# Optimization experiments

Measured on AMD Instinct MI355X. Metric: run time of the kernel, lower is better.

## Reference

```python
import jax, jax.numpy as jnp
import numpy as np
from jax import lax

V_JOINTS = 25
N_SCALES = 13
C1 = 96
N_SEG = 50
EPS = 1e-5

# NTU RGB+D 25-joint skeleton edges (0-indexed)
_EDGES = [(0,1),(1,20),(2,20),(3,2),(4,20),(5,4),(6,5),(7,6),(8,20),(9,8),
          (10,9),(11,10),(12,0),(13,12),(14,13),(15,14),(16,0),(17,16),
          (18,17),(19,18),(21,22),(22,7),(23,24),(24,11)]


def _build_A_powers():
    # MS-G3D disentangled multi-scale adjacency: k-hop shells, D^-1/2 A D^-1/2 normalized
    A = np.zeros((V_JOINTS, V_JOINTS), dtype=np.float64)
    for i, j in _EDGES:
        A[i, j] = 1.0
        A[j, i] = 1.0
    I = np.eye(V_JOINTS)
    mats = []
    for k in range(N_SCALES):
        if k == 0:
            Ak = I.copy()
        else:
            Ak = (np.minimum(np.linalg.matrix_power(A + I, k), 1)
                  - np.minimum(np.linalg.matrix_power(A + I, k - 1), 1))
            Ak = Ak + I  # with_self=True
        d = Ak.sum(-1)
        Dinv = np.diag(d ** -0.5)
        mats.append(Dinv @ Ak @ Dinv)
    return np.concatenate(mats, axis=0).astype(np.float32)  # (13*25, 25)


def _segments(T, n_seg):
    # Segment boundaries exactly as the torch code: int(round(linspace(1, T, n_seg+1)))
    t_vec = [int(round(v)) for v in np.linspace(1, T, n_seg + 1)]
    lens = [t_vec[i + 1] - t_vec[i] for i in range(n_seg)]
    L = max(lens)
    idx = np.zeros((n_seg, L), dtype=np.int32)
    mask = np.zeros((n_seg, L), dtype=np.float32)
    for s in range(n_seg):
        start = t_vec[s] - 1
        for l in range(L):
            idx[s, l] = min(start + l, T - 2)
            mask[s, l] = 1.0 if l < lens[s] else 0.0
    sp_idx = np.array([t - 1 for t in t_vec[:-1]], dtype=np.int32)
    return idx, mask, sp_idx


def setup_inputs() -> dict:
    key = jax.random.key(0)
    ks = jax.random.split(key, 18)
    N, M, C, T, V = 4, 2, 3, 300, V_JOINTS
    num_classes = 60
    Cbn = M * C * V                       # 150
    Dlog = C1 + C1 * (C1 - 1) // 2        # 4656 (depth-2 logsig dims)
    Din = C1 + Dlog                       # 4752 (start pos + logsig)
    f = lambda k, s: jax.random.normal(k, s, dtype=jnp.float32)
    return {
        'x': f(ks[0], (N, M, C, T, V)),
        'bn_g': 1.0 + 0.1 * f(ks[1], (Cbn,)),
        'bn_b': 0.1 * f(ks[2], (Cbn,)),
        'bn_m': 0.1 * f(ks[3], (Cbn,)),
        'bn_v': jax.random.uniform(ks[4], (Cbn,), minval=0.5, maxval=1.5),
        'A_powers': jnp.asarray(_build_A_powers()),
        'A_res': jax.random.uniform(ks[5], (N_SCALES * V, V), minval=-1e-6, maxval=1e-6),
        'W_gcn': f(ks[6], (C1, N_SCALES * C)) / np.sqrt(N_SCALES * C),
        'b_gcn': 0.1 * f(ks[7], (C1,)),
        'bn2_g': 1.0 + 0.1 * f(ks[8], (C1,)),
        'bn2_b': 0.1 * f(ks[9], (C1,)),
        'bn2_m': 0.1 * f(ks[10], (C1,)),
        'bn2_v': jax.random.uniform(ks[11], (C1,), minval=0.5, maxval=1.5),
        'W_ih': f(ks[12], (4 * C1, Din)) / np.sqrt(Din),
        'W_hh': f(ks[13], (4 * C1, C1)) / np.sqrt(C1),
        'b_ih': 0.1 * f(ks[14], (4 * C1,)),
        'b_hh': 0.1 * f(ks[15], (4 * C1,)),
        'W_fc': f(ks[16], (num_classes, C1)) / np.sqrt(C1),
        'b_fc': 0.1 * f(ks[17], (num_classes,)),
    }


def reference(x, bn_g, bn_b, bn_m, bn_v, A_powers, A_res, W_gcn, b_gcn,
              bn2_g, bn2_b, bn2_m, bn2_v, W_ih, W_hh, b_ih, b_hh, W_fc, b_fc):
    N, M, C, T, V = x.shape
    NM = N * M
    # --- data_bn (inference BatchNorm1d over M*V*C channels) ---
    xb = x.transpose(0, 1, 4, 2, 3).reshape(N, M * V * C, T)
    xb = (xb - bn_m[:, None]) * (bn_g / jnp.sqrt(bn_v + EPS))[:, None] + bn_b[:, None]
    xg = xb.reshape(NM, V, C, T).transpose(0, 2, 3, 1)          # (NM, C, T, V)
    # --- MS_GCN: multi-scale disentangled graph conv ---
    A = A_powers + A_res                                        # (S*V, V)
    sup = jnp.einsum('vu,nctu->nctv', A, xg)                    # (NM, C, T, S*V)
    sup = sup.reshape(NM, C, T, N_SCALES, V).transpose(0, 3, 1, 2, 4)
    sup = sup.reshape(NM, N_SCALES * C, T, V)
    y = jnp.einsum('oc,nctv->notv', W_gcn, sup) + b_gcn[None, :, None, None]
    y = (y - bn2_m[None, :, None, None]) * (bn2_g / jnp.sqrt(bn2_v + EPS))[None, :, None, None] \
        + bn2_b[None, :, None, None]
    y = jax.nn.relu(y)                                          # (NM, C1, T, V)
    # --- LogSigRNN: per-joint temporal path, depth-2 log-signature per segment ---
    p = y.transpose(0, 3, 2, 1).reshape(NM * V, T, C1)          # (B, T, C1)
    idx, mask, sp_idx = _segments(T, N_SEG)
    dx = jnp.diff(p, axis=1)                                    # (B, T-1, C1)
    dseg = dx[:, idx] * mask[None, :, :, None]                  # (B, nseg, L, C1)
    pseg = jnp.cumsum(dseg, axis=2) - dseg                      # exclusive prefix within segment
    s1 = dseg.sum(axis=2)                                       # level-1: total increment
    Q = jnp.einsum('bslc,bsld->bscd', pseg, dseg)               # (B, nseg, C1, C1)
    levy = 0.5 * (Q - jnp.swapaxes(Q, -1, -2))                  # level-2 (Levy area)
    iu, ju = np.triu_indices(C1, 1)
    ls2 = levy[:, :, iu, ju]                                    # (B, nseg, 4560)
    start_pos = p[:, sp_idx, :]                                 # (B, nseg, C1)
    feat = jnp.concatenate([start_pos, s1, ls2], axis=-1)       # (B, nseg, 4752)
    # --- LSTM (torch gate order i,f,g,o) ---
    B = feat.shape[0]
    xw = jnp.einsum('btd,gd->btg', feat, W_ih) + (b_ih + b_hh)
    def step(carry, xt):
        h, c = carry
        g = xt + h @ W_hh.T
        i, fg, gg, o = jnp.split(g, 4, axis=-1)
        c = jax.nn.sigmoid(fg) * c + jax.nn.sigmoid(i) * jnp.tanh(gg)
        h = jax.nn.sigmoid(o) * jnp.tanh(c)
        return (h, c), h
    h0 = jnp.zeros((B, C1), feat.dtype)
    _, hs = lax.scan(step, (h0, h0), jnp.swapaxes(xw, 0, 1))
    hs = jnp.swapaxes(hs, 0, 1)                                 # (B, nseg, C1)
    out = hs.reshape(NM, V, N_SEG, C1).transpose(0, 3, 2, 1)    # (NM, C1, nseg, V)
    out = out.reshape(N, M, C1, -1).mean(axis=3).mean(axis=1)   # (N, C1)
    return out @ W_fc.T + b_fc
```

## Files before the change

kernel.cpp:

```cpp
#include <hip/hip_runtime.h>
#include <math.h>

#define KF 4752
#define KP 4768
#define KSTEPS 149
#define G4 384
#define NPAIR 4560
#define EPSBN 1e-5f
#define XWHALF 3840000

typedef float f32x4 __attribute__((ext_vector_type(4)));
typedef short s16x8 __attribute__((ext_vector_type(8)));

__device__ __forceinline__ unsigned short f2bf(float x){
  unsigned u = __float_as_uint(x);
  return (unsigned short)((u + 0x7fffu + ((u>>16)&1u)) >> 16);
}
__device__ __forceinline__ float bf2f(unsigned short h){
  return __uint_as_float(((unsigned)h)<<16);
}

__device__ __forceinline__ int seg_start(int s){ return (s<=24)? 6*s : 149 + 6*(s-25); }
__device__ __forceinline__ int seg_len(int s){ return (s==24)?5:6; }

__global__ void kGeff(const float* bn_g, const float* bn_v,
                      const float* Ap, const float* Ar, const float* Wg,
                      const float* bn2_g, const float* bn2_v, float* geffT){
  int idx = blockIdx.x*256 + threadIdx.x;
  if (idx >= 2*96*25*75) return;
  int cu = idx % 75; int rest = idx/75;
  int v = rest % 25; rest /= 25;
  int o = rest % 96; int m = rest / 96;
  int c = cu/25, u = cu%25;
  int ch = (m*25+u)*3 + c;
  float s1 = bn_g[ch] / sqrtf(bn_v[ch] + EPSBN);
  float s2 = bn2_g[o] / sqrtf(bn2_v[o] + EPSBN);
  float acc = 0.f;
  for (int k=0;k<13;k++){
    float a = Ap[(k*25+v)*25+u] + Ar[(k*25+v)*25+u];
    acc += Wg[o*39 + k*3 + c] * a;
  }
  geffT[((size_t)(m*75+cu))*2400 + v*96 + o] = acc * s1 * s2;
}

__global__ __launch_bounds__(256) void kBeff(const float* bn_g,const float* bn_b,const float* bn_m,const float* bn_v,
                      const float* Ap,const float* Ar,const float* Wg,const float* bg,
                      const float* bn2_g,const float* bn2_b,const float* bn2_m,const float* bn2_v,
                      float* beffT){
  int wid  = (blockIdx.x*256 + threadIdx.x) >> 6;
  int lane = threadIdx.x & 63;
  if (wid >= 2*96*25) return;
  int v = wid % 25; int rest = wid/25; int o = rest % 96; int m = rest/96;
  float acc = 0.f;
  #pragma unroll
  for (int it=0; it<16; ++it){
    int item = it*64 + lane;
    if (item < 975){
      int k = item / 75; int cu = item % 75; int c = cu/25, u = cu%25;
      int ch = (m*25+u)*3 + c;
      float s1 = bn_g[ch] / sqrtf(bn_v[ch] + EPSBN);
      float t1 = bn_b[ch] - bn_m[ch]*s1;
      float a  = Ap[(k*25+v)*25+u] + Ar[(k*25+v)*25+u];
      acc += Wg[o*39 + k*3 + c] * a * t1;
    }
  }
  #pragma unroll
  for (int off=32; off; off>>=1) acc += __shfl_down(acc, off);
  if (lane == 0){
    acc += bg[o];
    float s2 = bn2_g[o]/sqrtf(bn2_v[o]+EPSBN);
    beffT[m*2400 + v*96 + o] = s2*(acc - bn2_m[o]) + bn2_b[o];
  }
}

__global__ void kPairs(int* pairs){
  int k = blockIdx.x*256+threadIdx.x;
  if (k >= NPAIR) return;
  int i=0, rem=k;
  while (rem >= 95 - i){ rem -= (95 - i); i++; }
  int j = i + 1 + rem;
  pairs[k] = (i<<7) | j;
}

__global__ void kWsplit(const float* w, unsigned short* whi, unsigned short* wlo){
  int idx = blockIdx.x*256 + threadIdx.x;
  if (idx >= G4*KP) return;
  int g = idx / KP, k = idx % KP;
  float v = (k < KF) ? w[(size_t)g*KF + k] : 0.f;
  unsigned short h = f2bf(v);
  whi[idx] = h;
  wlo[idx] = f2bf(v - bf2f(h));
}

#define TTILE 10
__global__ __launch_bounds__(256) void kP(const float* x, const float* geffT, const float* beffT, float* p){
  int nm = blockIdx.y;
  int t0 = blockIdx.x * TTILE;
  int m  = nm % 2;
  __shared__ float xs[75*TTILE];
  int tid = threadIdx.x;
  for (int li = tid; li < 75*TTILE; li += 256){
    int u = li % 25; int rest = li/25; int tt = rest % TTILE; int c = rest / TTILE;
    xs[(c*25+u)*TTILE + tt] = x[(((size_t)nm*3 + c)*300 + (t0+tt))*25 + u];
  }
  __syncthreads();
  const float* gT = geffT + (size_t)m*75*2400;
  for (int ow = tid; ow < 2400; ow += 256){
    int o = ow % 96, v = ow / 96;
    float b = beffT[m*2400 + ow];
    float acc[TTILE];
    #pragma unroll
    for (int t=0;t<TTILE;t++) acc[t] = b;
    for (int cu=0; cu<75; cu++){
      float gv = gT[(size_t)cu*2400 + ow];
      #pragma unroll
      for (int t=0;t<TTILE;t++) acc[t] += gv * xs[cu*TTILE+t];
    }
    #pragma unroll
    for (int t=0;t<TTILE;t++)
      p[((size_t)(nm*25+v)*300 + t0+t)*96 + o] = fmaxf(acc[t], 0.f);
  }
}

__global__ __launch_bounds__(256) void kFeat(const float* p, const int* pairs,
                                             unsigned short* fhi, unsigned short* flo, int row0){
  int row = row0 + blockIdx.x;
  int b = row / 50, s = row % 50;
  int S = seg_start(s), len = seg_len(s);
  __shared__ float ps[6][96];
  __shared__ float ds[6][96];
  int tid = threadIdx.x;
  size_t base = (size_t)blockIdx.x * KP;
  if (tid < 96){
    int c = tid;
    float pv[7];
    #pragma unroll
    for (int l=0;l<7;l++) pv[l] = p[((size_t)b*300 + S + l)*96 + c];
    float run = 0.f;
    #pragma unroll
    for (int l=0;l<6;l++){
      float d = (l < len) ? (pv[l+1]-pv[l]) : 0.f;
      ps[l][c] = run; ds[l][c] = d; run += d;
    }
    unsigned short h0 = f2bf(pv[0]);
    fhi[base + c] = h0; flo[base + c] = f2bf(pv[0] - bf2f(h0));
    unsigned short h1 = f2bf(run);
    fhi[base + 96 + c] = h1; flo[base + 96 + c] = f2bf(run - bf2f(h1));
  } else if (tid < 112){
    int c = KF + (tid - 96);
    fhi[base + c] = 0; flo[base + c] = 0;
  }
  __syncthreads();
  for (int k = tid; k < NPAIR; k += 256){
    int pr = pairs[k];
    int i = pr >> 7, j = pr & 127;
    float q = 0.f;
    #pragma unroll
    for (int l=0;l<6;l++) q += ps[l][i]*ds[l][j] - ps[l][j]*ds[l][i];
    q *= 0.5f;
    unsigned short h = f2bf(q);
    fhi[base + 192 + k] = h; flo[base + 192 + k] = f2bf(q - bf2f(h));
  }
}

__device__ __forceinline__ void gload16(const void* g, void* l){
  __builtin_amdgcn_global_load_lds(
      (const __attribute__((address_space(1))) void*)g,
      (__attribute__((address_space(3))) void*)l, 16, 0, 0);
}

__global__ __launch_bounds__(256) void kGemm(
    const unsigned short* __restrict__ fhi, const unsigned short* __restrict__ flo,
    const unsigned short* __restrict__ whi, const unsigned short* __restrict__ wlo,
    float* __restrict__ xw, int chunkRow0, int nrows)
{
  __shared__ unsigned short lds[2][20480];
  int tid  = threadIdx.x;
  int lane = tid & 63, w = tid >> 6;
  int colBase = blockIdx.x * 192;
  int zz      = blockIdx.y;
  int mblk    = blockIdx.z;
  int zbase   = zz * 75;
  int zSteps  = zz ? (KSTEPS - 75) : 75;

  const unsigned short* gptr[10];
  int ldsOff[10];
  #pragma unroll
  for (int q=0;q<10;q++){
    int c = (w*10 + q)*64 + lane;
    const unsigned short* bp; int rr;
    if (c < 512)        { rr = c;        bp = fhi + (size_t)(mblk*128 + (rr>>2))*KP; }
    else if (c < 1024)  { rr = c-512;    bp = flo + (size_t)(mblk*128 + (rr>>2))*KP; }
    else if (c < 1792)  { rr = c-1024;   bp = whi + (size_t)(colBase  + (rr>>2))*KP; }
    else                { rr = c-1792;   bp = wlo + (size_t)(colBase  + (rr>>2))*KP; }
    int row = rr>>2, gl = rr&3;
    int gs = gl ^ ((row>>1)&3);
    gptr[q]  = bp + gs*8;
    ldsOff[q] = (w*10 + q)*512;
  }

  int wm = w & 1, wn = w >> 1;
  int gsel = lane >> 4;
  int aoff[4], boff[6];
  #pragma unroll
  for (int fm=0; fm<4; fm++){
    int r = wm*64 + fm*16 + (lane&15);
    aoff[fm] = r*32 + ((gsel ^ ((r>>1)&3))*8);
  }
  #pragma unroll
  for (int fn=0; fn<6; fn++){
    int r = wn*96 + fn*16 + (lane&15);
    boff[fn] = 8192 + r*32 + ((gsel ^ ((r>>1)&3))*8);
  }

  f32x4 acc[4][6];
  #pragma unroll
  for (int fm=0;fm<4;fm++)
    #pragma unroll
    for (int fn=0;fn<6;fn++) acc[fm][fn] = (f32x4){0.f,0.f,0.f,0.f};

  #pragma unroll
  for (int q=0;q<10;q++) gload16(gptr[q] + (size_t)zbase*32, &lds[0][ldsOff[q]]);

  int cur = 0;
  for (int t=0; t<zSteps; ++t){
    __syncthreads();
    if (t+1 < zSteps){
      size_t ko = (size_t)(zbase + t + 1)*32;
      #pragma unroll
      for (int q=0;q<10;q++) gload16(gptr[q] + ko, &lds[cur^1][ldsOff[q]]);
    }
    const unsigned short* L = lds[cur];
    s16x8 ah[4], al[4], bh[6], bl[6];
    #pragma unroll
    for (int fm=0;fm<4;fm++){
      ah[fm] = *(const s16x8*)(L + aoff[fm]);
      al[fm] = *(const s16x8*)(L + aoff[fm] + 4096);
    }
    #pragma unroll
    for (int fn=0;fn<6;fn++){
      bh[fn] = *(const s16x8*)(L + boff[fn]);
      bl[fn] = *(const s16x8*)(L + boff[fn] + 6144);
    }
    #pragma unroll
    for (int fm=0;fm<4;fm++)
      #pragma unroll
      for (int fn=0;fn<6;fn++){
        acc[fm][fn] = __builtin_amdgcn_mfma_f32_16x16x32_bf16(ah[fm], bh[fn], acc[fm][fn], 0,0,0);
        acc[fm][fn] = __builtin_amdgcn_mfma_f32_16x16x32_bf16(ah[fm], bl[fn], acc[fm][fn], 0,0,0);
        acc[fm][fn] = __builtin_amdgcn_mfma_f32_16x16x32_bf16(al[fm], bh[fn], acc[fm][fn], 0,0,0);
      }
    cur ^= 1;
  }

  int rl = (lane>>4)*4, cl = lane&15;
  float* outp = xw + (size_t)zz*XWHALF;
  #pragma unroll
  for (int fm=0;fm<4;fm++){
    #pragma unroll
    for (int fn=0;fn<6;fn++){
      int gr0 = mblk*128 + wm*64 + fm*16 + rl;
      int gc  = colBase + wn*96 + fn*16 + cl;
      f32x4 v = acc[fm][fn];
      #pragma unroll
      for (int r=0;r<4;r++){
        int gr = gr0 + r;
        if (gr < nrows)
          outp[(size_t)(chunkRow0 + gr)*G4 + gc] = v[r];
      }
    }
  }
}

__global__ __launch_bounds__(384) void kLstm(const float* xw, const float* whh,
                                             const float* bih, const float* bhh, float* hsum){
  int b = blockIdx.x;
  int g = threadIdx.x;
  __shared__ __align__(16) float h_s[96];
  __shared__ float gbuf[384];
  float wreg[96];
  #pragma unroll
  for (int k=0;k<96;k++) wreg[k] = whh[(size_t)g*96 + k];
  float breg = bih[g] + bhh[g];
  float cval = 0.f, hacc = 0.f;
  if (g < 96) h_s[g] = 0.f;
  __syncthreads();
  const float* xrow  = xw + (size_t)b*50*G4;
  const float* xrow2 = xrow + XWHALF;
  for (int t=0;t<50;t++){
    float acc = xrow[t*G4 + g] + xrow2[t*G4 + g] + breg;
    #pragma unroll
    for (int k=0;k<96;k+=4){
      float4 h4 = *(const float4*)&h_s[k];
      acc += wreg[k]*h4.x + wreg[k+1]*h4.y + wreg[k+2]*h4.z + wreg[k+3]*h4.w;
    }
    gbuf[g] = acc;
    __syncthreads();
    if (g < 96){
      float ig = gbuf[g], fg = gbuf[96+g], gg = gbuf[192+g], og = gbuf[288+g];
      float si = 1.f/(1.f+expf(-ig));
      float sf = 1.f/(1.f+expf(-fg));
      float so = 1.f/(1.f+expf(-og));
      cval = sf*cval + si*tanhf(gg);
      float h = so * tanhf(cval);
      h_s[g] = h;
      hacc += h;
    }
    __syncthreads();
  }
  if (g < 96) hsum[(size_t)b*96 + g] = hacc;
}

__global__ void kOut(const float* hsum, const float* wfc, const float* bfc, float* out){
  int n = blockIdx.x;
  __shared__ float pool[96];
  int tid = threadIdx.x;
  if (tid < 96){
    float a = 0.f;
    for (int mv=0; mv<50; mv++) a += hsum[((size_t)(n*50 + mv))*96 + tid];
    pool[tid] = a / 2500.f;
  }
  __syncthreads();
  if (tid < 60){
    float a = bfc[tid];
    for (int o=0;o<96;o++) a += pool[o]*wfc[tid*96+o];
    out[n*60+tid] = a;
  }
}

extern "C" void kernel_launch(void* const* d_in, const int* in_sizes, int n_in,
                              void* d_out, int out_size, void* d_ws, size_t ws_size,
                              hipStream_t stream){
  const float* x     = (const float*)d_in[0];
  const float* bn_g  = (const float*)d_in[1];
  const float* bn_b  = (const float*)d_in[2];
  const float* bn_m  = (const float*)d_in[3];
  const float* bn_v  = (const float*)d_in[4];
  const float* Ap    = (const float*)d_in[5];
  const float* Ar    = (const float*)d_in[6];
  const float* Wg    = (const float*)d_in[7];
  const float* bg    = (const float*)d_in[8];
  const float* bn2_g = (const float*)d_in[9];
  const float* bn2_b = (const float*)d_in[10];
  const float* bn2_m = (const float*)d_in[11];
  const float* bn2_v = (const float*)d_in[12];
  const float* wih   = (const float*)d_in[13];
  const float* whh   = (const float*)d_in[14];
  const float* bih   = (const float*)d_in[15];
  const float* bhh   = (const float*)d_in[16];
  const float* wfc   = (const float*)d_in[17];
  const float* bfc   = (const float*)d_in[18];
  float* out = (float*)d_out;

  float* ws    = (float*)d_ws;
  float* geffT = ws;
  float* beffT = geffT + 360000;
  int*   pairs = (int*)(beffT + 4800);
  float* pbuf  = beffT + 4800 + 4560;
  float* xw    = pbuf + 5760000;
  float* hsum  = xw + 2*XWHALF;
  unsigned short* whiP = (unsigned short*)(hsum + 19200);
  unsigned short* wloP = whiP + (size_t)G4*KP;
  unsigned short* fhi  = wloP + (size_t)G4*KP;
  size_t fixedFloats = 360000u + 4800u + 4560u + 5760000u + 2u*XWHALF + 19200u
                     + (size_t)G4*KP;
  long long availB = (long long)ws_size - (long long)(fixedFloats*4);
  long long perBlk128 = 128LL*KP*2*2;
  int blocks128 = (availB > 0) ? (int)(availB / perBlk128) : 1;
  if (blocks128 < 1)  blocks128 = 1;
  if (blocks128 > 79) blocks128 = 79;
  int chunkRows = blocks128 * 128;
  unsigned short* flo = fhi + (size_t)chunkRows*KP;

  kGeff<<<(2*96*25*75 + 255)/256, 256, 0, stream>>>(bn_g, bn_v, Ap, Ar, Wg, bn2_g, bn2_v, geffT);
  kBeff<<<1200, 256, 0, stream>>>(bn_g, bn_b, bn_m, bn_v, Ap, Ar, Wg, bg,
                                  bn2_g, bn2_b, bn2_m, bn2_v, beffT);
  kPairs<<<(NPAIR + 255)/256, 256, 0, stream>>>(pairs);
  kWsplit<<<((G4*KP) + 255)/256, 256, 0, stream>>>(wih, whiP, wloP);
  kP<<<dim3(30, 8), 256, 0, stream>>>(x, geffT, beffT, pbuf);

  for (int r0 = 0; r0 < 10000; r0 += chunkRows){
    int nr = 10000 - r0; if (nr > chunkRows) nr = chunkRows;
    kFeat<<<nr, 256, 0, stream>>>(pbuf, pairs, fhi, flo, r0);
    kGemm<<<dim3(2, 2, (nr + 127)/128), 256, 0, stream>>>(fhi, flo, whiP, wloP, xw, r0, nr);
  }

  kLstm<<<200, 384, 0, stream>>>(xw, whh, bih, bhh, hsum);
  kOut<<<4, 128, 0, stream>>>(hsum, wfc, bfc, out);
}
```

Measured before the change: 397.7 us.

## Enlarge GEMM M-tile, remap blocks to XCDs, fuse prep kernels, vectorize feature writes

```diff
diff --git a/kernel.cpp b/kernel.cpp
--- a/kernel.cpp
+++ b/kernel.cpp
@@ -23,73 +23,76 @@
 __device__ __forceinline__ int seg_start(int s){ return (s<=24)? 6*s : 149 + 6*(s-25); }
 __device__ __forceinline__ int seg_len(int s){ return (s==24)?5:6; }
 
-__global__ void kGeff(const float* bn_g, const float* bn_v,
-                      const float* Ap, const float* Ar, const float* Wg,
-                      const float* bn2_g, const float* bn2_v, float* geffT){
-  int idx = blockIdx.x*256 + threadIdx.x;
-  if (idx >= 2*96*25*75) return;
-  int cu = idx % 75; int rest = idx/75;
-  int v = rest % 25; rest /= 25;
-  int o = rest % 96; int m = rest / 96;
-  int c = cu/25, u = cu%25;
-  int ch = (m*25+u)*3 + c;
-  float s1 = bn_g[ch] / sqrtf(bn_v[ch] + EPSBN);
-  float s2 = bn2_g[o] / sqrtf(bn2_v[o] + EPSBN);
-  float acc = 0.f;
-  for (int k=0;k<13;k++){
-    float a = Ap[(k*25+v)*25+u] + Ar[(k*25+v)*25+u];
-    acc += Wg[o*39 + k*3 + c] * a;
-  }
-  geffT[((size_t)(m*75+cu))*2400 + v*96 + o] = acc * s1 * s2;
-}
-
-__global__ __launch_bounds__(256) void kBeff(const float* bn_g,const float* bn_b,const float* bn_m,const float* bn_v,
-                      const float* Ap,const float* Ar,const float* Wg,const float* bg,
-                      const float* bn2_g,const float* bn2_b,const float* bn2_m,const float* bn2_v,
-                      float* beffT){
-  int wid  = (blockIdx.x*256 + threadIdx.x) >> 6;
-  int lane = threadIdx.x & 63;
-  if (wid >= 2*96*25) return;
-  int v = wid % 25; int rest = wid/25; int o = rest % 96; int m = rest/96;
-  float acc = 0.f;
-  #pragma unroll
-  for (int it=0; it<16; ++it){
-    int item = it*64 + lane;
-    if (item < 975){
-      int k = item / 75; int cu = item % 75; int c = cu/25, u = cu%25;
-      int ch = (m*25+u)*3 + c;
-      float s1 = bn_g[ch] / sqrtf(bn_v[ch] + EPSBN);
-      float t1 = bn_b[ch] - bn_m[ch]*s1;
-      float a  = Ap[(k*25+v)*25+u] + Ar[(k*25+v)*25+u];
-      acc += Wg[o*39 + k*3 + c] * a * t1;
-    }
-  }
-  #pragma unroll
-  for (int off=32; off; off>>=1) acc += __shfl_down(acc, off);
-  if (lane == 0){
-    acc += bg[o];
-    float s2 = bn2_g[o]/sqrtf(bn2_v[o]+EPSBN);
-    beffT[m*2400 + v*96 + o] = s2*(acc - bn2_m[o]) + bn2_b[o];
-  }
-}
-
-__global__ void kPairs(int* pairs){
-  int k = blockIdx.x*256+threadIdx.x;
-  if (k >= NPAIR) return;
-  int i=0, rem=k;
-  while (rem >= 95 - i){ rem -= (95 - i); i++; }
-  int j = i + 1 + rem;
-  pairs[k] = (i<<7) | j;
-}
-
-__global__ void kWsplit(const float* w, unsigned short* whi, unsigned short* wlo){
-  int idx = blockIdx.x*256 + threadIdx.x;
-  if (idx >= G4*KP) return;
-  int g = idx / KP, k = idx % KP;
-  float v = (k < KF) ? w[(size_t)g*KF + k] : 0.f;
-  unsigned short h = f2bf(v);
-  whi[idx] = h;
-  wlo[idx] = f2bf(v - bf2f(h));
+#define NB_GEFF 1407
+#define NB_BEFF 1200
+#define NB_PAIR 18
+#define NB_WSPL 7152
+
+__global__ __launch_bounds__(256) void kPre(
+    const float* bn_g,const float* bn_b,const float* bn_m,const float* bn_v,
+    const float* Ap,const float* Ar,const float* Wg,const float* bg,
+    const float* bn2_g,const float* bn2_b,const float* bn2_m,const float* bn2_v,
+    const float* wih,
+    float* geffT, float* beffT, int* pairs, unsigned short* whi, unsigned short* wlo)
+{
+  int bid = blockIdx.x, tid = threadIdx.x;
+  if (bid < NB_GEFF){
+    int idx = bid*256 + tid;
+    if (idx >= 2*96*25*75) return;
+    int cu = idx % 75; int rest = idx/75;
+    int v = rest % 25; rest /= 25;
+    int o = rest % 96; int m = rest / 96;
+    int c = cu/25, u = cu%25;
+    int ch = (m*25+u)*3 + c;
+    float s1 = bn_g[ch] / sqrtf(bn_v[ch] + EPSBN);
+    float s2 = bn2_g[o] / sqrtf(bn2_v[o] + EPSBN);
+    float acc = 0.f;
+    for (int k=0;k<13;k++){
+      float a = Ap[(k*25+v)*25+u] + Ar[(k*25+v)*25+u];
+      acc += Wg[o*39 + k*3 + c] * a;
+    }
+    geffT[((size_t)(m*75+cu))*2400 + v*96 + o] = acc * s1 * s2;
+  } else if (bid < NB_GEFF + NB_BEFF){
+    int wid  = ((bid-NB_GEFF)*256 + tid) >> 6;
+    int lane = tid & 63;
+    if (wid >= 2*96*25) return;
+    int v = wid % 25; int rest = wid/25; int o = rest % 96; int m = rest/96;
+    float acc = 0.f;
+    #pragma unroll
+    for (int it=0; it<16; ++it){
+      int item = it*64 + lane;
+      if (item < 975){
+        int k = item / 75; int cu = item % 75; int c = cu/25, u = cu%25;
+        int ch = (m*25+u)*3 + c;
+        float s1 = bn_g[ch] / sqrtf(bn_v[ch] + EPSBN);
+        float t1 = bn_b[ch] - bn_m[ch]*s1;
+        float a  = Ap[(k*25+v)*25+u] + Ar[(k*25+v)*25+u];
+        acc += Wg[o*39 + k*3 + c] * a * t1;
+      }
+    }
+    #pragma unroll
+    for (int off=32; off; off>>=1) acc += __shfl_down(acc, off);
+    if (lane == 0){
+      acc += bg[o];
+      float s2 = bn2_g[o]/sqrtf(bn2_v[o]+EPSBN);
+      beffT[m*2400 + v*96 + o] = s2*(acc - bn2_m[o]) + bn2_b[o];
+    }
+  } else if (bid < NB_GEFF + NB_BEFF + NB_PAIR){
+    int k = (bid - NB_GEFF - NB_BEFF)*256 + tid;
+    if (k >= NPAIR) return;
+    int i=0, rem=k;
+    while (rem >= 95 - i){ rem -= (95 - i); i++; }
+    int j = i + 1 + rem;
+    pairs[k] = (i<<7) | j;
+  } else {
+    int idx = (bid - NB_GEFF - NB_BEFF - NB_PAIR)*256 + tid;
+    if (idx >= G4*KP) return;
+    int g = idx / KP, k = idx % KP;
+    float v = (k < KF) ? wih[(size_t)g*KF + k] : 0.f;
+    unsigned short h = f2bf(v);
+    whi[idx] = h;
+    wlo[idx] = f2bf(v - bf2f(h));
+  }
 }
 
 #define TTILE 10
@@ -127,8 +130,8 @@
   int row = row0 + blockIdx.x;
   int b = row / 50, s = row % 50;
   int S = seg_start(s), len = seg_len(s);
-  __shared__ float ps[6][96];
-  __shared__ float ds[6][96];
+  __shared__ float ps8[96][12];
+  __shared__ float ds8[96][12];
   int tid = threadIdx.x;
   size_t base = (size_t)blockIdx.x * KP;
   if (tid < 96){
@@ -140,8 +143,9 @@
     #pragma unroll
     for (int l=0;l<6;l++){
       float d = (l < len) ? (pv[l+1]-pv[l]) : 0.f;
-      ps[l][c] = run; ds[l][c] = d; run += d;
-    }
+      ps8[c][l] = run; ds8[c][l] = d; run += d;
+    }
+    ps8[c][6] = 0.f; ps8[c][7] = 0.f; ds8[c][6] = 0.f; ds8[c][7] = 0.f;
     unsigned short h0 = f2bf(pv[0]);
     fhi[base + c] = h0; flo[base + c] = f2bf(pv[0] - bf2f(h0));
     unsigned short h1 = f2bf(run);
@@ -151,15 +155,32 @@
     fhi[base + c] = 0; flo[base + c] = 0;
   }
   __syncthreads();
-  for (int k = tid; k < NPAIR; k += 256){
-    int pr = pairs[k];
-    int i = pr >> 7, j = pr & 127;
-    float q = 0.f;
-    #pragma unroll
-    for (int l=0;l<6;l++) q += ps[l][i]*ds[l][j] - ps[l][j]*ds[l][i];
-    q *= 0.5f;
-    unsigned short h = f2bf(q);
-    fhi[base + 192 + k] = h; flo[base + 192 + k] = f2bf(q - bf2f(h));
+  for (int g8 = tid; g8 < NPAIR/8; g8 += 256){
+    int k0 = g8*8;
+    s16x8 vh, vl;
+    int icur = -1;
+    f32x4 pi0={0,0,0,0}, pi1={0,0,0,0}, di0={0,0,0,0}, di1={0,0,0,0};
+    #pragma unroll
+    for (int e=0;e<8;e++){
+      int pr = pairs[k0+e]; int i = pr>>7, j = pr&127;
+      if (i != icur){
+        icur = i;
+        pi0 = *(const f32x4*)&ps8[i][0]; pi1 = *(const f32x4*)&ps8[i][4];
+        di0 = *(const f32x4*)&ds8[i][0]; di1 = *(const f32x4*)&ds8[i][4];
+      }
+      f32x4 pj0 = *(const f32x4*)&ps8[j][0], pj1 = *(const f32x4*)&ps8[j][4];
+      f32x4 dj0 = *(const f32x4*)&ds8[j][0], dj1 = *(const f32x4*)&ds8[j][4];
+      float q = pi0.x*dj0.x + pi0.y*dj0.y + pi0.z*dj0.z + pi0.w*dj0.w
+              + pi1.x*dj1.x + pi1.y*dj1.y
+              - pj0.x*di0.x - pj0.y*di0.y - pj0.z*di0.z - pj0.w*di0.w
+              - pj1.x*di1.x - pj1.y*di1.y;
+      q *= 0.5f;
+      unsigned short h = f2bf(q);
+      vh[e] = (short)h;
+      vl[e] = (short)f2bf(q - bf2f(h));
+    }
+    *(s16x8*)(fhi + base + 192 + k0) = vh;
+    *(s16x8*)(flo + base + 192 + k0) = vl;
   }
 }
 
@@ -172,94 +193,99 @@
 __global__ __launch_bounds__(256) void kGemm(
     const unsigned short* __restrict__ fhi, const unsigned short* __restrict__ flo,
     const unsigned short* __restrict__ whi, const unsigned short* __restrict__ wlo,
-    float* __restrict__ xw, int chunkRow0, int nrows)
+    float* __restrict__ xw, int chunkRow0, int nrows, int nmblk)
 {
-  __shared__ unsigned short lds[2][20480];
+  __shared__ unsigned short lds[2][28672];
   int tid  = threadIdx.x;
   int lane = tid & 63, w = tid >> 6;
-  int colBase = blockIdx.x * 192;
-  int zz      = blockIdx.y;
-  int mblk    = blockIdx.z;
-  int zbase   = zz * 75;
-  int zSteps  = zz ? (KSTEPS - 75) : 75;
-
-  const unsigned short* gptr[10];
-  int ldsOff[10];
-  #pragma unroll
-  for (int q=0;q<10;q++){
-    int c = (w*10 + q)*64 + lane;
-    const unsigned short* bp; int rr;
-    if (c < 512)        { rr = c;        bp = fhi + (size_t)(mblk*128 + (rr>>2))*KP; }
-    else if (c < 1024)  { rr = c-512;    bp = flo + (size_t)(mblk*128 + (rr>>2))*KP; }
-    else if (c < 1792)  { rr = c-1024;   bp = whi + (size_t)(colBase  + (rr>>2))*KP; }
-    else                { rr = c-1792;   bp = wlo + (size_t)(colBase  + (rr>>2))*KP; }
-    int row = rr>>2, gl = rr&3;
-    int gs = gl ^ ((row>>1)&3);
-    gptr[q]  = bp + gs*8;
-    ldsOff[q] = (w*10 + q)*512;
+  int id = blockIdx.x;
+  int col, zz, mblk;
+  if (nmblk == 40){
+    int xcd = id & 7, rank = id >> 3, s2 = rank >> 1;
+    col = rank & 1;
+    int pp = s2*8 + xcd;
+    mblk = pp >> 1; zz = pp & 1;
+  } else { col = id & 1; zz = (id >> 1) & 1; mblk = id >> 2; }
+  int rowBase = mblk*256, colBase = col*192;
+  int zbase = zz*75, zSteps = zz ? 74 : 75;
+
+  int off[14];
+  #pragma unroll
+  for (int q=0;q<14;q++){
+    int c = q*256 + tid;
+    int rr = (q<4) ? c : (q<8) ? c-1024 : (q<11) ? c-2048 : c-2816;
+    int rw = rr>>2, gl = rr&3;
+    int gs = gl ^ ((rw>>1)&3);
+    int grow = (q<8) ? (rowBase + rw) : (colBase + rw);
+    off[q] = grow*KP + gs*8;
   }
 
   int wm = w & 1, wn = w >> 1;
-  int gsel = lane >> 4;
-  int aoff[4], boff[6];
-  #pragma unroll
-  for (int fm=0; fm<4; fm++){
-    int r = wm*64 + fm*16 + (lane&15);
+  int gsel = lane >> 4, li = lane & 15;
+  int aoff[8], boff[6];
+  #pragma unroll
+  for (int fm=0; fm<8; fm++){
+    int r = wm*128 + fm*16 + li;
     aoff[fm] = r*32 + ((gsel ^ ((r>>1)&3))*8);
   }
   #pragma unroll
   for (int fn=0; fn<6; fn++){
-    int r = wn*96 + fn*16 + (lane&15);
-    boff[fn] = 8192 + r*32 + ((gsel ^ ((r>>1)&3))*8);
-  }
-
-  f32x4 acc[4][6];
-  #pragma unroll
-  for (int fm=0;fm<4;fm++)
+    int r = wn*96 + fn*16 + li;
+    boff[fn] = 16384 + r*32 + ((gsel ^ ((r>>1)&3))*8);
+  }
+
+  f32x4 acc[8][6];
+  #pragma unroll
+  for (int fm=0;fm<8;fm++)
     #pragma unroll
     for (int fn=0;fn<6;fn++) acc[fm][fn] = (f32x4){0.f,0.f,0.f,0.f};
 
-  #pragma unroll
-  for (int q=0;q<10;q++) gload16(gptr[q] + (size_t)zbase*32, &lds[0][ldsOff[q]]);
-
-  int cur = 0;
-  for (int t=0; t<zSteps; ++t){
-    __syncthreads();
-    if (t+1 < zSteps){
-      size_t ko = (size_t)(zbase + t + 1)*32;
-      #pragma unroll
-      for (int q=0;q<10;q++) gload16(gptr[q] + ko, &lds[cur^1][ldsOff[q]]);
-    }
-    const unsigned short* L = lds[cur];
-    s16x8 ah[4], al[4], bh[6], bl[6];
-    #pragma unroll
-    for (int fm=0;fm<4;fm++){
-      ah[fm] = *(const s16x8*)(L + aoff[fm]);
-      al[fm] = *(const s16x8*)(L + aoff[fm] + 4096);
-    }
-    #pragma unroll
-    for (int fn=0;fn<6;fn++){
-      bh[fn] = *(const s16x8*)(L + boff[fn]);
-      bl[fn] = *(const s16x8*)(L + boff[fn] + 6144);
-    }
-    #pragma unroll
-    for (int fm=0;fm<4;fm++)
-      #pragma unroll
-      for (int fn=0;fn<6;fn++){
-        acc[fm][fn] = __builtin_amdgcn_mfma_f32_16x16x32_bf16(ah[fm], bh[fn], acc[fm][fn], 0,0,0);
-        acc[fm][fn] = __builtin_amdgcn_mfma_f32_16x16x32_bf16(ah[fm], bl[fn], acc[fm][fn], 0,0,0);
-        acc[fm][fn] = __builtin_amdgcn_mfma_f32_16x16x32_bf16(al[fm], bh[fn], acc[fm][fn], 0,0,0);
-      }
-    cur ^= 1;
-  }
+#define STAGE(BUF, T) { \
+    int ko = (zbase + (T))*32; \
+    _Pragma("unroll") \
+    for (int q=0;q<14;q++){ \
+      const unsigned short* bp = (q<4)?fhi:(q<8)?flo:(q<11)?whi:wlo; \
+      gload16(bp + (size_t)(off[q] + ko), &lds[BUF][q*2048 + w*512]); \
+    } }
+
+#define COMPUTE(BI) { \
+    const unsigned short* L = lds[BI]; \
+    s16x8 bh[6], bl[6]; \
+    _Pragma("unroll") \
+    for (int fn=0;fn<6;fn++){ \
+      bh[fn] = *(const s16x8*)(L + boff[fn]); \
+      bl[fn] = *(const s16x8*)(L + boff[fn] + 6144); \
+    } \
+    _Pragma("unroll") \
+    for (int fm=0;fm<8;fm++){ \
+      s16x8 ah = *(const s16x8*)(L + aoff[fm]); \
+      s16x8 al = *(const s16x8*)(L + aoff[fm] + 8192); \
+      _Pragma("unroll") \
+      for (int fn=0;fn<6;fn++){ \
+        acc[fm][fn] = __builtin_amdgcn_mfma_f32_16x16x32_bf16(ah, bh[fn], acc[fm][fn], 0,0,0); \
+        acc[fm][fn] = __builtin_amdgcn_mfma_f32_16x16x32_bf16(ah, bl[fn], acc[fm][fn], 0,0,0); \
+        acc[fm][fn] = __builtin_amdgcn_mfma_f32_16x16x32_bf16(al, bh[fn], acc[fm][fn], 0,0,0); \
+      } \
+    } }
+
+  STAGE(0, 0);
+  for (int t=0; t<zSteps-1; ++t){
+    __builtin_amdgcn_s_barrier();
+    STAGE((t+1)&1, t+1);
+    asm volatile("s_waitcnt vmcnt(14)" ::: "memory");
+    COMPUTE(t&1);
+  }
+  __builtin_amdgcn_s_barrier();
+  asm volatile("s_waitcnt vmcnt(0)" ::: "memory");
+  COMPUTE((zSteps-1)&1);
 
   int rl = (lane>>4)*4, cl = lane&15;
   float* outp = xw + (size_t)zz*XWHALF;
   #pragma unroll
-  for (int fm=0;fm<4;fm++){
+  for (int fm=0;fm<8;fm++){
     #pragma unroll
     for (int fn=0;fn<6;fn++){
-      int gr0 = mblk*128 + wm*64 + fm*16 + rl;
+      int gr0 = rowBase + wm*128 + fm*16 + rl;
       int gc  = colBase + wn*96 + fn*16 + cl;
       f32x4 v = acc[fm][fn];
       #pragma unroll
@@ -270,45 +296,52 @@
       }
     }
   }
-}
-
-__global__ __launch_bounds__(384) void kLstm(const float* xw, const float* whh,
+#undef STAGE
+#undef COMPUTE
+}
+
+__global__ __launch_bounds__(192) void kLstm(const float* xw, const float* whh,
                                              const float* bih, const float* bhh, float* hsum){
   int b = blockIdx.x;
-  int g = threadIdx.x;
+  int t = threadIdx.x;
+  int gA = t;
+  int gB = t + 192;
   __shared__ __align__(16) float h_s[96];
   __shared__ float gbuf[384];
-  float wreg[96];
-  #pragma unroll
-  for (int k=0;k<96;k++) wreg[k] = whh[(size_t)g*96 + k];
-  float breg = bih[g] + bhh[g];
+  float wA[96], wB[96];
+  #pragma unroll
+  for (int k=0;k<96;k++){ wA[k] = whh[(size_t)gA*96 + k]; wB[k] = whh[(size_t)gB*96 + k]; }
+  float bA = bih[gA] + bhh[gA];
+  float bB = bih[gB] + bhh[gB];
   float cval = 0.f, hacc = 0.f;
-  if (g < 96) h_s[g] = 0.f;
+  if (t < 96) h_s[t] = 0.f;
   __syncthreads();
-  const float* xrow  = xw + (size_t)b*50*G4;
-  const float* xrow2 = xrow + XWHALF;
-  for (int t=0;t<50;t++){
-    float acc = xrow[t*G4 + g] + xrow2[t*G4 + g] + breg;
+  const float* xr = xw + (size_t)b*50*G4;
+  for (int st=0; st<50; st++){
+    int o = st*G4;
+    float aA = xr[o+gA] + xr[XWHALF+o+gA] + bA;
+    float aB = xr[o+gB] + xr[XWHALF+o+gB] + bB;
     #pragma unroll
     for (int k=0;k<96;k+=4){
       float4 h4 = *(const float4*)&h_s[k];
-      acc += wreg[k]*h4.x + wreg[k+1]*h4.y + wreg[k+2]*h4.z + wreg[k+3]*h4.w;
-    }
-    gbuf[g] = acc;
+      aA += wA[k]*h4.x + wA[k+1]*h4.y + wA[k+2]*h4.z + wA[k+3]*h4.w;
+      aB += wB[k]*h4.x + wB[k+1]*h4.y + wB[k+2]*h4.z + wB[k+3]*h4.w;
+    }
+    gbuf[gA] = aA; gbuf[gB] = aB;
     __syncthreads();
-    if (g < 96){
-      float ig = gbuf[g], fg = gbuf[96+g], gg = gbuf[192+g], og = gbuf[288+g];
+    if (t < 96){
+      float ig = gbuf[t], fg = gbuf[96+t], gg = gbuf[192+t], og = gbuf[288+t];
       float si = 1.f/(1.f+expf(-ig));
       float sf = 1.f/(1.f+expf(-fg));
       float so = 1.f/(1.f+expf(-og));
       cval = sf*cval + si*tanhf(gg);
       float h = so * tanhf(cval);
-      h_s[g] = h;
+      h_s[t] = h;
       hacc += h;
     }
     __syncthreads();
   }
-  if (g < 96) hsum[(size_t)b*96 + g] = hacc;
+  if (t < 96) hsum[(size_t)b*96 + t] = hacc;
 }
 
 __global__ void kOut(const float* hsum, const float* wfc, const float* bfc, float* out){
@@ -358,33 +391,32 @@
   int*   pairs = (int*)(beffT + 4800);
   float* pbuf  = beffT + 4800 + 4560;
   float* xw    = pbuf + 5760000;
-  float* hsum  = xw + 2*XWHALF;
+  float* hsum  = xw + 2*(size_t)XWHALF;
   unsigned short* whiP = (unsigned short*)(hsum + 19200);
   unsigned short* wloP = whiP + (size_t)G4*KP;
   unsigned short* fhi  = wloP + (size_t)G4*KP;
-  size_t fixedFloats = 360000u + 4800u + 4560u + 5760000u + 2u*XWHALF + 19200u
+  size_t fixedFloats = 360000u + 4800u + 4560u + 5760000u + 2u*(size_t)XWHALF + 19200u
                      + (size_t)G4*KP;
   long long availB = (long long)ws_size - (long long)(fixedFloats*4);
-  long long perBlk128 = 128LL*KP*2*2;
-  int blocks128 = (availB > 0) ? (int)(availB / perBlk128) : 1;
-  if (blocks128 < 1)  blocks128 = 1;
-  if (blocks128 > 79) blocks128 = 79;
-  int chunkRows = blocks128 * 128;
-  unsigned short* flo = fhi + (size_t)chunkRows*KP;
-
-  kGeff<<<(2*96*25*75 + 255)/256, 256, 0, stream>>>(bn_g, bn_v, Ap, Ar, Wg, bn2_g, bn2_v, geffT);
-  kBeff<<<1200, 256, 0, stream>>>(bn_g, bn_b, bn_m, bn_v, Ap, Ar, Wg, bg,
-                                  bn2_g, bn2_b, bn2_m, bn2_v, beffT);
-  kPairs<<<(NPAIR + 255)/256, 256, 0, stream>>>(pairs);
-  kWsplit<<<((G4*KP) + 255)/256, 256, 0, stream>>>(wih, whiP, wloP);
+  long long perUnit = 256LL*KP*4;
+  long long units = (availB > 0) ? availB/perUnit : 1;
+  if (units < 1)  units = 1;
+  if (units > 40) units = 40;
+  int chunk = (int)units * 256;
+  unsigned short* flo = fhi + (size_t)chunk*KP;
+
+  kPre<<<NB_GEFF+NB_BEFF+NB_PAIR+NB_WSPL, 256, 0, stream>>>(
+      bn_g, bn_b, bn_m, bn_v, Ap, Ar, Wg, bg, bn2_g, bn2_b, bn2_m, bn2_v,
+      wih, geffT, beffT, pairs, whiP, wloP);
   kP<<<dim3(30, 8), 256, 0, stream>>>(x, geffT, beffT, pbuf);
 
-  for (int r0 = 0; r0 < 10000; r0 += chunkRows){
-    int nr = 10000 - r0; if (nr > chunkRows) nr = chunkRows;
+  for (int r0 = 0; r0 < 10000; r0 += chunk){
+    int nr = 10000 - r0; if (nr > chunk) nr = chunk;
     kFeat<<<nr, 256, 0, stream>>>(pbuf, pairs, fhi, flo, r0);
-    kGemm<<<dim3(2, 2, (nr + 127)/128), 256, 0, stream>>>(fhi, flo, whiP, wloP, xw, r0, nr);
-  }
-
-  kLstm<<<200, 384, 0, stream>>>(xw, whh, bih, bhh, hsum);
+    int mblkc = (nr + 255)/256;
+    kGemm<<<4*mblkc, 256, 0, stream>>>(fhi, flo, whiP, wloP, xw, r0, nr, mblkc);
+  }
+
+  kLstm<<<200, 192, 0, stream>>>(xw, whh, bih, bhh, hsum);
   kOut<<<4, 128, 0, stream>>>(hsum, wfc, bfc, out);
 }
```

New measurement: 476.1 us. 1.2x slower.
